# Kernel optimization log

Hardware: AMD Instinct MI355X
Metric: run time of the kernel (lower is better)

Reference implementation:

```python
import jax, jax.numpy as jnp
import numpy as np
from jax import lax

WIN_SIZE = 11
SIGMA = 1.5
K1, K2 = 0.01, 0.03
DATA_RANGE = 1.0


def _gauss_1d(size=WIN_SIZE, sigma=SIGMA):
    coords = jnp.arange(size, dtype=jnp.float32) - size // 2
    g = jnp.exp(-(coords ** 2) / (2.0 * sigma ** 2))
    return g / jnp.sum(g)


def _blur(x, win):
    # x: (1, C, H, W); separable depthwise gaussian, VALID padding (pytorch_msssim)
    C = x.shape[1]
    dn = ('NCHW', 'OIHW', 'NCHW')
    kw = jnp.tile(win.reshape(1, 1, 1, -1), (C, 1, 1, 1))  # (C,1,1,K)
    kh = jnp.tile(win.reshape(1, 1, -1, 1), (C, 1, 1, 1))  # (C,1,K,1)
    x = lax.conv_general_dilated(x, kw, (1, 1), 'VALID',
                                 dimension_numbers=dn, feature_group_count=C)
    x = lax.conv_general_dilated(x, kh, (1, 1), 'VALID',
                                 dimension_numbers=dn, feature_group_count=C)
    return x


def _ssim_loss(pred, targ, height, width):
    x = pred.reshape(1, 3, height, width)
    y = targ.reshape(1, 3, height, width)
    win = _gauss_1d()
    C1 = (K1 * DATA_RANGE) ** 2
    C2 = (K2 * DATA_RANGE) ** 2

    mu1 = _blur(x, win)
    mu2 = _blur(y, win)
    mu1_sq = mu1 * mu1
    mu2_sq = mu2 * mu2
    mu1_mu2 = mu1 * mu2
    sigma1_sq = _blur(x * x, win) - mu1_sq
    sigma2_sq = _blur(y * y, win) - mu2_sq
    sigma12 = _blur(x * y, win) - mu1_mu2

    cs_map = (2.0 * sigma12 + C2) / (sigma1_sq + sigma2_sq + C2)
    ssim_map = ((2.0 * mu1_mu2 + C1) / (mu1_sq + mu2_sq + C1)) * cs_map
    return 1.0 - jnp.mean(ssim_map)


def setup_inputs() -> dict:
    key = jax.random.key(0)
    k1, k2 = jax.random.split(key)
    H, W = 2048, 2048
    return {
        'predicted_img': jax.random.uniform(k1, (1, 3, H, W), dtype=jnp.float32),
        'target_img': jax.random.uniform(k2, (1, 3, H, W), dtype=jnp.float32),
        'height': H,
        'width': W,
    }


def reference(predicted_img, target_img, height, width):
    return _ssim_loss(predicted_img, target_img, height, width)
```

## Files before the change

### kernel.cpp

```cpp
#include <hip/hip_runtime.h>
#include <math.h>

typedef float f32x2 __attribute__((ext_vector_type(2)));
typedef float f32x4 __attribute__((ext_vector_type(4)));

#define HH    2048
#define WW    2048
#define NCH   3
#define NOUT  2038
#define OWID  64
#define OH    128
#define CROWS 16
#define BUF   28
#define HAW   66
#define HCW   68
#define NTX   32
#define NTY   16
#define NBLOCKS (NTX*NTY*NCH)
#define NOUT_TOTAL 12460332.0f

__device__ __forceinline__ float ssim_term(float mu1, float mu2,
                                           float b11, float b22, float b12) {
    const float c1v = 1e-4f, c2v = 9e-4f;
    float mu1sq = mu1 * mu1;
    float mu2sq = mu2 * mu2;
    float mu12  = mu1 * mu2;
    float s11 = b11 - mu1sq;
    float s22 = b22 - mu2sq;
    float s12 = b12 - mu12;
    float csn = 2.f * s12 + c2v;
    float csd = s11 + s22 + c2v;
    float ln  = 2.f * mu12 + c1v;
    float ld  = mu1sq + mu2sq + c1v;
    return (csn * ln) * __builtin_amdgcn_rcpf(csd * ld);
}

__global__ __launch_bounds__(256, 2)
void ssim_main(const float* __restrict__ x, const float* __restrict__ y,
               float* __restrict__ partials) {
    __shared__ f32x2 hbA[BUF][HAW];
    __shared__ f32x2 hbB[BUF][HAW];
    __shared__ float hbC[BUF][HCW];
    __shared__ float wsum[4];

    const int tid = threadIdx.x;
    const int gx0 = blockIdx.x * OWID;
    const int gy0 = blockIdx.y * OH;
    const float* xb = x + (size_t)blockIdx.z * HH * WW;
    const float* yb = y + (size_t)blockIdx.z * HH * WW;

    float w[11];
    {
        float s = 0.f;
        #pragma unroll
        for (int i = 0; i < 11; ++i) {
            float d = (float)(i - 5);
            w[i] = expf(-d * d / 4.5f);
            s += w[i];
        }
        float inv = 1.f / s;
        #pragma unroll
        for (int i = 0; i < 11; ++i) w[i] *= inv;
    }

    const int lr  = tid >> 4;
    const int c0  = (tid & 15) * 4;
    const int gxc = gx0 + c0;

    f32x4 px[3], py[3];
    f32x2 px3, py3;

    auto PF = [&](int base) {
        int gy = gy0 + base + lr; if (gy > HH - 1) gy = HH - 1;
        const float* xr = xb + (size_t)gy * WW;
        const float* yr = yb + (size_t)gy * WW;
        #pragma unroll
        for (int a = 0; a < 3; ++a) {
            int g = gxc + 4 * a;
            if (g + 4 <= WW) {
                px[a] = *(const f32x4*)(xr + g);
                py[a] = *(const f32x4*)(yr + g);
            } else {
                int g0 = g     < WW ? g     : WW - 1;
                int g1 = g + 1 < WW ? g + 1 : WW - 1;
                int g2 = g + 2 < WW ? g + 2 : WW - 1;
                int g3 = g + 3 < WW ? g + 3 : WW - 1;
                px[a] = (f32x4){xr[g0], xr[g1], xr[g2], xr[g3]};
                py[a] = (f32x4){yr[g0], yr[g1], yr[g2], yr[g3]};
            }
        }
        {
            int g = gxc + 12;
            if (g + 2 <= WW) {
                px3 = *(const f32x2*)(xr + g);
                py3 = *(const f32x2*)(yr + g);
            } else {
                int g0 = g     < WW ? g     : WW - 1;
                int g1 = g + 1 < WW ? g + 1 : WW - 1;
                px3 = (f32x2){xr[g0], xr[g1]};
                py3 = (f32x2){yr[g0], yr[g1]};
            }
        }
    };

    auto BLUR = [&](int base, bool tailMask) {
        int slot = (base + lr) % BUF;
        f32x2 p[14];
        #pragma unroll
        for (int a = 0; a < 3; ++a)
            #pragma unroll
            for (int i = 0; i < 4; ++i)
                p[4 * a + i] = (f32x2){px[a][i], py[a][i]};
        p[12] = (f32x2){px3.x, py3.x};
        p[13] = (f32x2){px3.y, py3.y};
        f32x2 q[14]; float pr[14];
        #pragma unroll
        for (int t = 0; t < 14; ++t) {
            q[t]  = p[t] * p[t];
            pr[t] = p[t].x * p[t].y;
        }
        f32x2 hA[4] = {}, hB[4] = {};
        float hC[4] = {};
        #pragma unroll
        for (int k = 0; k < 11; ++k) {
            f32x2 wk2 = (f32x2){w[k], w[k]};
            #pragma unroll
            for (int j = 0; j < 4; ++j) {
                hA[j] = __builtin_elementwise_fma(wk2, p[j + k], hA[j]);
                hB[j] = __builtin_elementwise_fma(wk2, q[j + k], hB[j]);
                hC[j] = fmaf(w[k], pr[j + k], hC[j]);
            }
        }
        if (!tailMask || lr < 10) {
            *(f32x4*)&hbA[slot][c0]     = (f32x4){hA[0].x, hA[0].y, hA[1].x, hA[1].y};
            *(f32x4*)&hbA[slot][c0 + 2] = (f32x4){hA[2].x, hA[2].y, hA[3].x, hA[3].y};
            *(f32x4*)&hbB[slot][c0]     = (f32x4){hB[0].x, hB[0].y, hB[1].x, hB[1].y};
            *(f32x4*)&hbB[slot][c0 + 2] = (f32x4){hB[2].x, hB[2].y, hB[3].x, hB[3].y};
            *(float4*)&hbC[slot][c0]    = make_float4(hC[0], hC[1], hC[2], hC[3]);
        }
    };

    float partial = 0.f;

    PF(0);  BLUR(0, false);
    PF(16); BLUR(16, true);
    __syncthreads();

    const int col  = tid & 63;
    const int wid  = tid >> 6;
    const int ocol = gx0 + col;

    for (int m = 0; m < 8; ++m) {
        if (m < 7) PF(16 * m + 26);
        {
            const int r0 = 16 * m + wid * 4;
            int s = r0 % BUF;
            f32x2 aA[4] = {}, aB[4] = {};
            float aC[4] = {};
            #pragma unroll
            for (int j = 0; j < 14; ++j) {
                f32x2 va = hbA[s][col];
                f32x2 vb = hbB[s][col];
                float vc = hbC[s][col];
                #pragma unroll
                for (int i = 0; i < 4; ++i) {
                    const int k = j - i;
                    if (k >= 0 && k < 11) {
                        f32x2 wk2 = (f32x2){w[k], w[k]};
                        aA[i] = __builtin_elementwise_fma(wk2, va, aA[i]);
                        aB[i] = __builtin_elementwise_fma(wk2, vb, aB[i]);
                        aC[i] = fmaf(w[k], vc, aC[i]);
                    }
                }
                s = (s == BUF - 1) ? 0 : s + 1;
            }
            #pragma unroll
            for (int i = 0; i < 4; ++i) {
                int orow = gy0 + r0 + i;
                if (orow < NOUT && ocol < NOUT)
                    partial += ssim_term(aA[i].x, aA[i].y, aB[i].x, aB[i].y, aC[i]);
            }
        }
        __syncthreads();
        if (m < 7) {
            BLUR(16 * m + 26, false);
            __syncthreads();
        }
    }

    #pragma unroll
    for (int off = 32; off > 0; off >>= 1)
        partial += __shfl_down(partial, off, 64);
    if ((tid & 63) == 0) wsum[tid >> 6] = partial;
    __syncthreads();
    if (tid == 0) {
        int bid = (blockIdx.z * gridDim.y + blockIdx.y) * gridDim.x + blockIdx.x;
        partials[bid] = wsum[0] + wsum[1] + wsum[2] + wsum[3];
    }
}

__global__ __launch_bounds__(256)
void ssim_finalize(const float* __restrict__ partials, float* __restrict__ out) {
    __shared__ float ws[4];
    float s = 0.f;
    for (int i = threadIdx.x; i < NBLOCKS / 4; i += 256) {
        float4 v = ((const float4*)partials)[i];
        s += (v.x + v.y) + (v.z + v.w);
    }
    #pragma unroll
    for (int off = 32; off > 0; off >>= 1)
        s += __shfl_down(s, off, 64);
    if ((threadIdx.x & 63) == 0) ws[threadIdx.x >> 6] = s;
    __syncthreads();
    if (threadIdx.x == 0)
        out[0] = 1.f - (ws[0] + ws[1] + ws[2] + ws[3]) / NOUT_TOTAL;
}

extern "C" void kernel_launch(void* const* d_in, const int* in_sizes, int n_in,
                              void* d_out, int out_size, void* d_ws, size_t ws_size,
                              hipStream_t stream) {
    const float* x = (const float*)d_in[0];
    const float* y = (const float*)d_in[1];
    float* out = (float*)d_out;
    float* partials = (float*)d_ws;

    dim3 grid(NTX, NTY, NCH);
    ssim_main<<<grid, dim3(256), 0, stream>>>(x, y, partials);
    ssim_finalize<<<1, 256, 0, stream>>>(partials, out);
}
```

Before: 162.5 us.

## Split block into per-wave column strips with private LDS buffers, drop barriers

Each wavefront now handles its own 16-column strip with private LDS ring buffers for the horizontal blur results, so the block-wide __syncthreads between the horizontal and vertical passes are removed. This removes barrier stalls and lets waves progress independently. In exchange, each strip needs its own 10-column halo, so global loads and horizontal blur work per output rise substantially.

After: 156.2 us. 1.04x faster.

```diff
diff --git a/kernel.cpp b/kernel.cpp
--- a/kernel.cpp
+++ b/kernel.cpp
@@ -9,11 +9,12 @@
 #define NCH   3
 #define NOUT  2038
 #define OWID  64
+#define SW    16
 #define OH    128
 #define CROWS 16
 #define BUF   28
-#define HAW   66
-#define HCW   68
+#define APW   17
+#define CPW   18
 #define NTX   32
 #define NTY   16
 #define NBLOCKS (NTX*NTY*NCH)
@@ -38,14 +39,16 @@
 __global__ __launch_bounds__(256, 2)
 void ssim_main(const float* __restrict__ x, const float* __restrict__ y,
                float* __restrict__ partials) {
-    __shared__ f32x2 hbA[BUF][HAW];
-    __shared__ f32x2 hbB[BUF][HAW];
-    __shared__ float hbC[BUF][HCW];
+    __shared__ f32x2 hbA[4][BUF][APW];
+    __shared__ f32x2 hbB[4][BUF][APW];
+    __shared__ float hbC[4][BUF][CPW];
     __shared__ float wsum[4];
 
-    const int tid = threadIdx.x;
-    const int gx0 = blockIdx.x * OWID;
-    const int gy0 = blockIdx.y * OH;
+    const int tid  = threadIdx.x;
+    const int lane = tid & 63;
+    const int wid  = tid >> 6;
+    const int gx0  = blockIdx.x * OWID + wid * SW;
+    const int gy0  = blockIdx.y * OH;
     const float* xb = x + (size_t)blockIdx.z * HH * WW;
     const float* yb = y + (size_t)blockIdx.z * HH * WW;
 
@@ -63,8 +66,8 @@
         for (int i = 0; i < 11; ++i) w[i] *= inv;
     }
 
-    const int lr  = tid >> 4;
-    const int c0  = (tid & 15) * 4;
+    const int lr  = lane >> 2;
+    const int c0  = (lane & 3) * 4;
     const int gxc = gx0 + c0;
 
     f32x4 px[3], py[3];
@@ -132,60 +135,59 @@
             }
         }
         if (!tailMask || lr < 10) {
-            *(f32x4*)&hbA[slot][c0]     = (f32x4){hA[0].x, hA[0].y, hA[1].x, hA[1].y};
-            *(f32x4*)&hbA[slot][c0 + 2] = (f32x4){hA[2].x, hA[2].y, hA[3].x, hA[3].y};
-            *(f32x4*)&hbB[slot][c0]     = (f32x4){hB[0].x, hB[0].y, hB[1].x, hB[1].y};
-            *(f32x4*)&hbB[slot][c0 + 2] = (f32x4){hB[2].x, hB[2].y, hB[3].x, hB[3].y};
-            *(float4*)&hbC[slot][c0]    = make_float4(hC[0], hC[1], hC[2], hC[3]);
+            f32x2* rA = &hbA[wid][slot][c0];
+            f32x2* rB = &hbB[wid][slot][c0];
+            rA[0] = hA[0]; rA[1] = hA[1]; rA[2] = hA[2]; rA[3] = hA[3];
+            rB[0] = hB[0]; rB[1] = hB[1]; rB[2] = hB[2]; rB[3] = hB[3];
+            float* rC = &hbC[wid][slot][c0];
+            *(f32x2*)(rC)     = (f32x2){hC[0], hC[1]};
+            *(f32x2*)(rC + 2) = (f32x2){hC[2], hC[3]};
         }
     };
 
     float partial = 0.f;
+
+    const int cc   = lane & 15;
+    const int rg   = lane >> 4;
+    const int ocol = gx0 + cc;
+
+    auto CSTAGE = [&](int m) {
+        const int r0 = 16 * m + rg * 4;
+        int s = r0 % BUF;
+        f32x2 aA[4] = {}, aB[4] = {};
+        float aC[4] = {};
+        #pragma unroll
+        for (int j = 0; j < 14; ++j) {
+            f32x2 va = hbA[wid][s][cc];
+            f32x2 vb = hbB[wid][s][cc];
+            float vc = hbC[wid][s][cc];
+            #pragma unroll
+            for (int i = 0; i < 4; ++i) {
+                const int k = j - i;
+                if (k >= 0 && k < 11) {
+                    f32x2 wk2 = (f32x2){w[k], w[k]};
+                    aA[i] = __builtin_elementwise_fma(wk2, va, aA[i]);
+                    aB[i] = __builtin_elementwise_fma(wk2, vb, aB[i]);
+                    aC[i] = fmaf(w[k], vc, aC[i]);
+                }
+            }
+            s = (s == BUF - 1) ? 0 : s + 1;
+        }
+        #pragma unroll
+        for (int i = 0; i < 4; ++i) {
+            int orow = gy0 + r0 + i;
+            if (orow < NOUT && ocol < NOUT)
+                partial += ssim_term(aA[i].x, aA[i].y, aB[i].x, aB[i].y, aC[i]);
+        }
+    };
 
     PF(0);  BLUR(0, false);
     PF(16); BLUR(16, true);
-    __syncthreads();
-
-    const int col  = tid & 63;
-    const int wid  = tid >> 6;
-    const int ocol = gx0 + col;
 
     for (int m = 0; m < 8; ++m) {
         if (m < 7) PF(16 * m + 26);
-        {
-            const int r0 = 16 * m + wid * 4;
-            int s = r0 % BUF;
-            f32x2 aA[4] = {}, aB[4] = {};
-            float aC[4] = {};
-            #pragma unroll
-            for (int j = 0; j < 14; ++j) {
-                f32x2 va = hbA[s][col];
-                f32x2 vb = hbB[s][col];
-                float vc = hbC[s][col];
-                #pragma unroll
-                for (int i = 0; i < 4; ++i) {
-                    const int k = j - i;
-                    if (k >= 0 && k < 11) {
-                        f32x2 wk2 = (f32x2){w[k], w[k]};
-                        aA[i] = __builtin_elementwise_fma(wk2, va, aA[i]);
-                        aB[i] = __builtin_elementwise_fma(wk2, vb, aB[i]);
-                        aC[i] = fmaf(w[k], vc, aC[i]);
-                    }
-                }
-                s = (s == BUF - 1) ? 0 : s + 1;
-            }
-            #pragma unroll
-            for (int i = 0; i < 4; ++i) {
-                int orow = gy0 + r0 + i;
-                if (orow < NOUT && ocol < NOUT)
-                    partial += ssim_term(aA[i].x, aA[i].y, aB[i].x, aB[i].y, aC[i]);
-            }
-        }
-        __syncthreads();
-        if (m < 7) {
-            BLUR(16 * m + 26, false);
-            __syncthreads();
-        }
+        CSTAGE(m);
+        if (m < 7) BLUR(16 * m + 26, false);
     }
 
     #pragma unroll
```
